# Performance work log

Hardware: AMD Instinct MI355X
Metric: run time of the kernel (lower is better)

The kernel has to match this reference:

```python
import jax, jax.numpy as jnp
import numpy as np

jax.config.update("jax_enable_x64", True)  # torch lfilter runs in double precision

SR = 24000
RES_SIZE = 64
R_MIN, R_MAX = 0.9999, 0.99999
B, T = 4, 120000


def setup_inputs() -> dict:
    # Probe coefficients (fixed buffers, computed exactly as in Probe.__init__)
    theta_min = 2 * np.pi * 10.0 / SR
    theta_max = 2 * np.pi * 100.0 / SR
    theta = np.exp(np.linspace(np.log(theta_min), np.log(theta_max), RES_SIZE))
    radii = np.linspace(R_MIN, R_MAX, RES_SIZE)
    a1 = -2.0 * radii * np.cos(theta)          # [C]
    a2 = radii ** 2                             # [C]
    b0 = (1.0 - radii) * 0.5                    # [C]

    # Tank mixing weight: orthogonal init, shape [out=64, in=128] (rows orthonormal)
    rng = np.random.default_rng(1337)
    q, _ = np.linalg.qr(rng.standard_normal((2 * RES_SIZE, RES_SIZE)))  # [128,64], orthonormal cols
    W = q.T.astype(np.float32)                  # [64,128]

    key = jax.random.key(0)
    k1, k2 = jax.random.split(key)
    pred = jax.random.normal(k1, (B, 1, T), dtype=jnp.float32)
    target = jax.random.normal(k2, (B, 1, T), dtype=jnp.float32)
    return {
        "pred": pred,
        "target": target,
        "a1": jnp.asarray(a1, jnp.float64),
        "a2": jnp.asarray(a2, jnp.float64),
        "b0": jnp.asarray(b0, jnp.float64),
        "W": jnp.asarray(W, jnp.float32),
    }


def _biquad_bank(x, a1, a2, b0):
    """Biquad filter bank. x: [N, T] float64; coeffs: [C]. Returns [N, C, T].
    y[t] = b0*x[t] - a1*y[t-1] - a2*y[t-2]  (a0 = 1, b1 = b2 = 0, clamp=False)
    """
    n = x.shape[0]
    c = a1.shape[0]

    def step(carry, xt):
        y1, y2 = carry  # each [N, C]
        y = b0[None, :] * xt[:, None] - a1[None, :] * y1 - a2[None, :] * y2
        return (y, y1), y

    init = (jnp.zeros((n, c), x.dtype), jnp.zeros((n, c), x.dtype))
    _, ys = jax.lax.scan(step, init, x.T)      # [T, N, C]
    return jnp.transpose(ys, (1, 2, 0))        # [N, C, T]


def _probe(x, a1, a2, b0):
    """x: [B,1,T] float -> [B, 2C, T] float32 (fwd state ++ bwd state)."""
    xs = x[:, 0, :].astype(jnp.float64)        # [B, T]
    # run forward-time and reversed-time filters in one batched scan
    both = jnp.concatenate([xs, xs[:, ::-1]], axis=0)       # [2B, T]
    ys = _biquad_bank(both, a1, a2, b0)                      # [2B, C, T]
    nb = xs.shape[0]
    fwd_state = ys[:nb]                                      # [B, C, T]
    bwd_state = ys[nb:][:, :, ::-1]                          # [B, C, T] (flipped back)
    return jnp.concatenate([fwd_state, bwd_state], axis=1).astype(jnp.float32)


def _tank(x, W):
    """x: [B, 2C, T], W: [C, 2C] -> tanh(W @ x): [B, C, T]."""
    return jnp.tanh(jnp.einsum("bct,oc->bot", x, W))


def reference(pred, target, a1, a2, b0, W):
    t = pred.shape[-1]
    margin = t // 3
    p_emb = _tank(_probe(pred, a1, a2, b0), W)    # [B, C, T]
    t_emb = _tank(_probe(target, a1, a2, b0), W)  # [B, C, T]
    p_valid = p_emb[..., margin:t - margin]
    t_valid = t_emb[..., margin:t - margin]
    return jnp.mean(jnp.abs(p_valid - t_valid))
```

## Files before the change

### kernel.cpp

```cpp
#include <hip/hip_runtime.h>

#define T_LEN 120000
#define LBLK 160
#define PBLK 750
#define PB_USED 500
#define SEG_LEN 25
#define NSEG_USED 20
#define SEGC0 10
#define NSEGC 11
#define CCH 32
#define NCHUNK 5
#define BATCH 4
#define K0 250
#define NKV 250
#define DENOM 20480000.0
#define YSTR 130

typedef _Float16 half8 __attribute__((ext_vector_type(8)));
typedef float f32x4 __attribute__((ext_vector_type(4)));

__device__ __forceinline__ float fast_tanh(float x) {
  float e = __expf(2.0f * x);
  return 1.0f - 2.0f / (e + 1.0f);
}

__device__ __forceinline__ bool coeffs_are_f64(const void* a2p) {
  double probe = *(const double*)a2p;
  return probe > 0.9 && probe < 1.0;
}
__device__ __forceinline__ double coeff_d(const void* p, bool f64, int ch) {
  return f64 ? ((const double*)p)[ch] : (double)((const float*)p)[ch];
}

__device__ __forceinline__ void mat_pow(double A1, double A2, int e,
                                        double& r00, double& r01,
                                        double& r10, double& r11) {
  double m00 = -A1, m01 = -A2, m10 = 1.0, m11 = 0.0;
  r00 = 1.0; r01 = 0.0; r10 = 0.0; r11 = 1.0;
  while (e) {
    if (e & 1) {
      double t00 = r00 * m00 + r01 * m10, t01 = r00 * m01 + r01 * m11;
      double t10 = r10 * m00 + r11 * m10, t11 = r10 * m01 + r11 * m11;
      r00 = t00; r01 = t01; r10 = t10; r11 = t11;
    }
    e >>= 1;
    if (e) {
      double t00 = m00 * m00 + m01 * m10, t01 = m00 * m01 + m01 * m11;
      double t10 = m10 * m00 + m11 * m10, t11 = m10 * m01 + m11 * m11;
      m00 = t00; m01 = t01; m10 = t10; m11 = t11;
    }
  }
}

__global__ __launch_bounds__(256) void pass1(
    const float* __restrict__ pred, const float* __restrict__ tgt,
    const void* a1p, const void* a2p, const void* b0p,
    double* __restrict__ fbuf, double* __restrict__ wsum)
{
  if ((blockIdx.x | blockIdx.y) == 0 && threadIdx.x == 0) {
    wsum[0] = 0.0;
    ((unsigned int*)(wsum + 1))[0] = 0u;
  }
  int k = blockIdx.x;
  int g = threadIdx.x >> 6, lane = threadIdx.x & 63;
  int gu = __builtin_amdgcn_readfirstlane(g);
  int r = blockIdx.y * 4 + gu;
  int i = r >> 3, d = (r >> 2) & 1, b = r & 3;
  const float* sig = (i ? tgt : pred) + b * T_LEN;
  __shared__ float xs[4][LBLK];
  int base = k * LBLK;
  for (int j = lane; j < LBLK; j += 64)
    xs[gu][j] = d ? sig[T_LEN - 1 - (base + j)] : sig[base + j];
  __syncthreads();
  int ch = lane;
  bool f64 = coeffs_are_f64(a2p);
  float A1 = (float)coeff_d(a1p, f64, ch);
  float A2 = (float)coeff_d(a2p, f64, ch);
  float B0 = (float)coeff_d(b0p, f64, ch);
  float y1 = 0.0f, y2 = 0.0f;
  for (int j = 0; j < LBLK; ++j) {
    float y = fmaf(-A1, y1, fmaf(-A2, y2, B0 * xs[gu][j]));
    y2 = y1; y1 = y;
  }
  int s = r * 64 + ch;
  ((double2*)fbuf)[(size_t)k * 1024 + s] = make_double2((double)y1, (double)y2);
}

__global__ __launch_bounds__(64) void pass2a(
    const void* a1p, const void* a2p,
    const double* __restrict__ fbuf, double* __restrict__ sbuf,
    double* __restrict__ atab)
{
  int seg = blockIdx.x >> 4;
  int s = ((blockIdx.x & 15) << 6) + threadIdx.x;
  int ch = s & 63;
  bool f64 = coeffs_are_f64(a2p);
  double r00, r01, r10, r11;
  mat_pow(coeff_d(a1p, f64, ch), coeff_d(a2p, f64, ch), LBLK, r00, r01, r10, r11);
  const double2* fb = (const double2*)fbuf;
  double y1 = 0.0, y2 = 0.0;
  for (int jj = 0; jj < SEG_LEN / 5; ++jj) {
    size_t kb = (size_t)(seg * SEG_LEN + jj * 5) * 1024 + s;
    double2 f0 = fb[kb], f1 = fb[kb + 1024], f2 = fb[kb + 2048],
            f3 = fb[kb + 3072], f4 = fb[kb + 4096];
    double n1, n2;
    n1 = r00*y1 + r01*y2 + f0.x; n2 = r10*y1 + r11*y2 + f0.y; y1=n1; y2=n2;
    n1 = r00*y1 + r01*y2 + f1.x; n2 = r10*y1 + r11*y2 + f1.y; y1=n1; y2=n2;
    n1 = r00*y1 + r01*y2 + f2.x; n2 = r10*y1 + r11*y2 + f2.y; y1=n1; y2=n2;
    n1 = r00*y1 + r01*y2 + f3.x; n2 = r10*y1 + r11*y2 + f3.y; y1=n1; y2=n2;
    n1 = r00*y1 + r01*y2 + f4.x; n2 = r10*y1 + r11*y2 + f4.y; y1=n1; y2=n2;
  }
  ((double2*)sbuf)[(size_t)seg * 1024 + s] = make_double2(y1, y2);

  if (blockIdx.x == 0) {
    double p00 = 1.0, p01 = 0.0, p10 = 0.0, p11 = 1.0;
    double b00 = r00, b01 = r01, b10 = r10, b11 = r11;
    int e = SEG_LEN;
    while (e) {
      if (e & 1) {
        double t00 = p00*b00 + p01*b10, t01 = p00*b01 + p01*b11;
        double t10 = p10*b00 + p11*b10, t11 = p10*b01 + p11*b11;
        p00 = t00; p01 = t01; p10 = t10; p11 = t11;
      }
      e >>= 1;
      if (e) {
        double t00 = b00*b00 + b01*b10, t01 = b00*b01 + b01*b11;
        double t10 = b10*b00 + b11*b10, t11 = b10*b01 + b11*b11;
        b00 = t00; b01 = t01; b10 = t10; b11 = t11;
      }
    }
    double* ap = atab + ch * 8;
    ap[0] = r00; ap[1] = r01; ap[2] = r10; ap[3] = r11;
    ap[4] = p00; ap[5] = p01; ap[6] = p10; ap[7] = p11;
  }
}

__global__ __launch_bounds__(64) void pass2c(
    const double* __restrict__ fbuf, const double* __restrict__ sbuf,
    const double* __restrict__ atab, double* __restrict__ stbuf)
{
  int seg = SEGC0 + (blockIdx.x >> 4);
  int s = ((blockIdx.x & 15) << 6) + threadIdx.x;
  int ch = s & 63;
  const double2* ap = (const double2*)(atab + ch * 8);
  double2 ra = ap[0], rb = ap[1], qa = ap[2], qb = ap[3];
  double r00 = ra.x, r01 = ra.y, r10 = rb.x, r11 = rb.y;
  double q00 = qa.x, q01 = qa.y, q10 = qb.x, q11 = qb.y;

  double y1 = 0.0, y2 = 0.0;
  const double2* sb = (const double2*)sbuf;
  #pragma unroll 1
  for (int qq = 0; qq < NSEG_USED; qq += 5) {
    double2 f[5];
    #pragma unroll
    for (int p = 0; p < 5; ++p) f[p] = sb[(size_t)(qq + p) * 1024 + s];
    #pragma unroll
    for (int p = 0; p < 5; ++p) {
      if (qq + p < seg) {
        double n1 = q00 * y1 + q01 * y2 + f[p].x;
        double n2 = q10 * y1 + q11 * y2 + f[p].y;
        y1 = n1; y2 = n2;
      }
    }
  }

  const double2* fb = (const double2*)fbuf;
  double2* st = (double2*)stbuf;
  #pragma unroll 1
  for (int jb = 0; jb < SEG_LEN; jb += 5) {
    double2 fv[5];
    #pragma unroll
    for (int q = 0; q < 5; ++q) {
      int m = seg * SEG_LEN + jb + q;
      int mc = m < PB_USED ? m : PB_USED - 1;
      fv[q] = fb[(size_t)mc * 1024 + s];
    }
    #pragma unroll
    for (int q = 0; q < 5; ++q) {
      int m = seg * SEG_LEN + jb + q;
      if (m <= K0 + NKV) {
        st[(size_t)(m - K0) * 1024 + s] = make_double2(y1, y2);
        if (m < K0 + NKV) {
          double n1 = r00 * y1 + r01 * y2 + fv[q].x;
          double n2 = r10 * y1 + r11 * y2 + fv[q].y;
          y1 = n1; y2 = n2;
        }
      }
    }
  }
}

__global__ __launch_bounds__(256, 4) void pass3(
    const float* __restrict__ pred, const float* __restrict__ tgt,
    const void* a1p, const void* a2p, const void* b0p,
    const float* __restrict__ W, const double* __restrict__ stbuf,
    double* __restrict__ wsum, float* __restrict__ out)
{
  int k = K0 + blockIdx.x;
  int b = blockIdx.y;
  int tid = threadIdx.x;
  __shared__ __align__(16) _Float16 ys[2][64 * YSTR];
  __shared__ float red[4];

  int g = tid >> 6, lane = tid & 63;
  int gu = __builtin_amdgcn_readfirstlane(g);
  int iu = gu >> 1, du = gu & 1;
  int ch = lane;
  int n0 = gu * 16;
  int lm = lane & 15, quad = lane >> 4;

  bool f64 = coeffs_are_f64(a2p);
  double A1d = coeff_d(a1p, f64, ch), A2d = coeff_d(a2p, f64, ch);
  double B0d = coeff_d(b0p, f64, ch);
  float A1 = (float)A1d, A2 = (float)A2d, B0 = (float)B0d;
  float IA2 = (float)(1.0 / A2d);

  int m = du ? (PBLK - k) : k;
  int s = (iu * 8 + du * 4 + b) * 64 + ch;
  double2 v0 = ((const double2*)stbuf)[(size_t)(m - K0) * 1024 + s];
  float st0 = (float)v0.x, st1 = (float)v0.y;

  half8 wf[4][4];
  #pragma unroll
  for (int m0 = 0; m0 < 4; ++m0) {
    #pragma unroll
    for (int k0 = 0; k0 < 4; ++k0) {
      const float* wp = W + (m0 * 16 + lm) * 128 + k0 * 32 + quad * 8;
      float4 wa = *(const float4*)wp, wb = *(const float4*)(wp + 4);
      half8 h;
      h[0] = (_Float16)wa.x; h[1] = (_Float16)wa.y;
      h[2] = (_Float16)wa.z; h[3] = (_Float16)wa.w;
      h[4] = (_Float16)wb.x; h[5] = (_Float16)wb.y;
      h[6] = (_Float16)wb.z; h[7] = (_Float16)wb.w;
      wf[m0][k0] = h;
    }
  }

  const float* xp = (iu ? tgt : pred) + b * T_LEN + k * LBLK;

  float loss = 0.0f;
  for (int cc = 0; cc < NCHUNK; ++cc) {
    _Float16* yb = ys[cc & 1];
    if (du == 0) {
      #pragma unroll
      for (int tt = 0; tt < CCH; ++tt) {
        float x = xp[cc * CCH + tt];
        float y = fmaf(-A1, st0, fmaf(-A2, st1, B0 * x));
        yb[(2 * tt + iu) * YSTR + ch] = (_Float16)y;
        st1 = st0; st0 = y;
      }
    } else {
      #pragma unroll
      for (int tt = 0; tt < CCH; ++tt) {
        float x = xp[cc * CCH + tt];
        yb[(2 * tt + iu) * YSTR + 64 + ch] = (_Float16)st0;
        float ym2 = (fmaf(-A1, st1, B0 * x) - st0) * IA2;
        st0 = st1; st1 = ym2;
      }
    }
    __syncthreads();

    const _Float16* yrow = &yb[(n0 + lm) * YSTR + quad * 8];
    half8 bf0 = *(const half8*)(yrow);
    half8 bf1 = *(const half8*)(yrow + 32);
    half8 bf2 = *(const half8*)(yrow + 64);
    half8 bf3 = *(const half8*)(yrow + 96);
    #pragma unroll
    for (int m0 = 0; m0 < 4; ++m0) {
      f32x4 c = {0.f, 0.f, 0.f, 0.f};
      c = __builtin_amdgcn_mfma_f32_16x16x32_f16(wf[m0][0], bf0, c, 0, 0, 0);
      c = __builtin_amdgcn_mfma_f32_16x16x32_f16(wf[m0][1], bf1, c, 0, 0, 0);
      c = __builtin_amdgcn_mfma_f32_16x16x32_f16(wf[m0][2], bf2, c, 0, 0, 0);
      c = __builtin_amdgcn_mfma_f32_16x16x32_f16(wf[m0][3], bf3, c, 0, 0, 0);
      #pragma unroll
      for (int r = 0; r < 4; ++r) {
        float vv = fast_tanh(c[r]);
        float p = __shfl_xor(vv, 1);
        loss += fabsf(vv - p);
      }
    }
  }

  #pragma unroll
  for (int off = 32; off > 0; off >>= 1) loss += __shfl_down(loss, off);
  if (lane == 0) red[g] = loss;
  __syncthreads();
  if (tid == 0) {
    float blk = (red[0] + red[1]) + (red[2] + red[3]);
    atomicAdd(wsum, (double)blk);
    __threadfence();
    unsigned int n = atomicAdd((unsigned int*)(wsum + 1), 1u);
    if (n == (unsigned int)(NKV * BATCH - 1)) {
      __threadfence();
      double tot = atomicAdd(wsum, 0.0);
      out[0] = (float)(tot / DENOM);
    }
  }
}

extern "C" void kernel_launch(void* const* d_in, const int* in_sizes, int n_in,
                              void* d_out, int out_size, void* d_ws, size_t ws_size,
                              hipStream_t stream) {
  const float* pred = (const float*)d_in[0];
  const float* tgt  = (const float*)d_in[1];
  const void* a1p = d_in[2];
  const void* a2p = d_in[3];
  const void* b0p = d_in[4];
  const float* W  = (const float*)d_in[5];
  float* out = (float*)d_out;

  double* base = (double*)d_ws;
  double* wsum = base;
  double* fbuf = base + 8;
  double* sbuf = fbuf + (size_t)PB_USED * 1024 * 2;
  double* atab = sbuf + (size_t)32 * 1024 * 2;
  double* stbuf = atab + 512;

  pass1<<<dim3(PB_USED, 4), 256, 0, stream>>>(pred, tgt, a1p, a2p, b0p,
                                              fbuf, wsum);
  pass2a<<<NSEG_USED * 16, 64, 0, stream>>>(a1p, a2p, fbuf, sbuf, atab);
  pass2c<<<NSEGC * 16, 64, 0, stream>>>(fbuf, sbuf, atab, stbuf);
  pass3<<<dim3(NKV, BATCH), 256, 0, stream>>>(pred, tgt, a1p, a2p, b0p,
                                              W, stbuf, wsum, out);
}
```

Measured before the change: 128.7 us.

## Merge segment-scan passes and replace atomic loss reduction with finalize kernel

Removes the pass2a kernel that computed per-segment carries and the R^25 powers. pass2c now serially scans all block carries in its prefix (up to ~500 sequential steps per thread) using only the 160-step transition matrix, which removes one launch and the sbuf/atab traffic. The atomic accumulation with a last-block counter in pass3 is replaced by per-block partial sums written to memory and reduced by a separate single-block finalize kernel. The trade-off is a much longer serial dependency chain in pass2c and one extra kernel launch, in exchange for dropping one launch and the atomics.

```diff
diff --git a/kernel.cpp b/kernel.cpp
--- a/kernel.cpp
+++ b/kernel.cpp
@@ -5,7 +5,6 @@
 #define PBLK 750
 #define PB_USED 500
 #define SEG_LEN 25
-#define NSEG_USED 20
 #define SEGC0 10
 #define NSEGC 11
 #define CCH 32
@@ -55,12 +54,8 @@
 __global__ __launch_bounds__(256) void pass1(
     const float* __restrict__ pred, const float* __restrict__ tgt,
     const void* a1p, const void* a2p, const void* b0p,
-    double* __restrict__ fbuf, double* __restrict__ wsum)
-{
-  if ((blockIdx.x | blockIdx.y) == 0 && threadIdx.x == 0) {
-    wsum[0] = 0.0;
-    ((unsigned int*)(wsum + 1))[0] = 0u;
-  }
+    double* __restrict__ fbuf)
+{
   int k = blockIdx.x;
   int g = threadIdx.x >> 6, lane = threadIdx.x & 63;
   int gu = __builtin_amdgcn_readfirstlane(g);
@@ -86,101 +81,50 @@
   ((double2*)fbuf)[(size_t)k * 1024 + s] = make_double2((double)y1, (double)y2);
 }
 
-__global__ __launch_bounds__(64) void pass2a(
+__global__ __launch_bounds__(64) void pass2c(
     const void* a1p, const void* a2p,
-    const double* __restrict__ fbuf, double* __restrict__ sbuf,
-    double* __restrict__ atab)
-{
-  int seg = blockIdx.x >> 4;
+    const double* __restrict__ fbuf, double* __restrict__ stbuf)
+{
+  int seg = SEGC0 + (blockIdx.x >> 4);
   int s = ((blockIdx.x & 15) << 6) + threadIdx.x;
   int ch = s & 63;
   bool f64 = coeffs_are_f64(a2p);
   double r00, r01, r10, r11;
-  mat_pow(coeff_d(a1p, f64, ch), coeff_d(a2p, f64, ch), LBLK, r00, r01, r10, r11);
+  mat_pow(coeff_d(a1p, f64, ch), coeff_d(a2p, f64, ch), LBLK,
+          r00, r01, r10, r11);
   const double2* fb = (const double2*)fbuf;
+
   double y1 = 0.0, y2 = 0.0;
-  for (int jj = 0; jj < SEG_LEN / 5; ++jj) {
-    size_t kb = (size_t)(seg * SEG_LEN + jj * 5) * 1024 + s;
-    double2 f0 = fb[kb], f1 = fb[kb + 1024], f2 = fb[kb + 2048],
-            f3 = fb[kb + 3072], f4 = fb[kb + 4096];
-    double n1, n2;
-    n1 = r00*y1 + r01*y2 + f0.x; n2 = r10*y1 + r11*y2 + f0.y; y1=n1; y2=n2;
-    n1 = r00*y1 + r01*y2 + f1.x; n2 = r10*y1 + r11*y2 + f1.y; y1=n1; y2=n2;
-    n1 = r00*y1 + r01*y2 + f2.x; n2 = r10*y1 + r11*y2 + f2.y; y1=n1; y2=n2;
-    n1 = r00*y1 + r01*y2 + f3.x; n2 = r10*y1 + r11*y2 + f3.y; y1=n1; y2=n2;
-    n1 = r00*y1 + r01*y2 + f4.x; n2 = r10*y1 + r11*y2 + f4.y; y1=n1; y2=n2;
-  }
-  ((double2*)sbuf)[(size_t)seg * 1024 + s] = make_double2(y1, y2);
-
-  if (blockIdx.x == 0) {
-    double p00 = 1.0, p01 = 0.0, p10 = 0.0, p11 = 1.0;
-    double b00 = r00, b01 = r01, b10 = r10, b11 = r11;
-    int e = SEG_LEN;
-    while (e) {
-      if (e & 1) {
-        double t00 = p00*b00 + p01*b10, t01 = p00*b01 + p01*b11;
-        double t10 = p10*b00 + p11*b10, t11 = p10*b01 + p11*b11;
-        p00 = t00; p01 = t01; p10 = t10; p11 = t11;
-      }
-      e >>= 1;
-      if (e) {
-        double t00 = b00*b00 + b01*b10, t01 = b00*b01 + b01*b11;
-        double t10 = b10*b00 + b11*b10, t11 = b10*b01 + b11*b11;
-        b00 = t00; b01 = t01; b10 = t10; b11 = t11;
-      }
-    }
-    double* ap = atab + ch * 8;
-    ap[0] = r00; ap[1] = r01; ap[2] = r10; ap[3] = r11;
-    ap[4] = p00; ap[5] = p01; ap[6] = p10; ap[7] = p11;
-  }
-}
-
-__global__ __launch_bounds__(64) void pass2c(
-    const double* __restrict__ fbuf, const double* __restrict__ sbuf,
-    const double* __restrict__ atab, double* __restrict__ stbuf)
-{
-  int seg = SEGC0 + (blockIdx.x >> 4);
-  int s = ((blockIdx.x & 15) << 6) + threadIdx.x;
-  int ch = s & 63;
-  const double2* ap = (const double2*)(atab + ch * 8);
-  double2 ra = ap[0], rb = ap[1], qa = ap[2], qb = ap[3];
-  double r00 = ra.x, r01 = ra.y, r10 = rb.x, r11 = rb.y;
-  double q00 = qa.x, q01 = qa.y, q10 = qb.x, q11 = qb.y;
-
-  double y1 = 0.0, y2 = 0.0;
-  const double2* sb = (const double2*)sbuf;
+  int pref = seg * SEG_LEN;
   #pragma unroll 1
-  for (int qq = 0; qq < NSEG_USED; qq += 5) {
+  for (int mb = 0; mb < pref; mb += 5) {
     double2 f[5];
     #pragma unroll
-    for (int p = 0; p < 5; ++p) f[p] = sb[(size_t)(qq + p) * 1024 + s];
-    #pragma unroll
-    for (int p = 0; p < 5; ++p) {
-      if (qq + p < seg) {
-        double n1 = q00 * y1 + q01 * y2 + f[p].x;
-        double n2 = q10 * y1 + q11 * y2 + f[p].y;
-        y1 = n1; y2 = n2;
-      }
-    }
-  }
-
-  const double2* fb = (const double2*)fbuf;
+    for (int q = 0; q < 5; ++q) f[q] = fb[(size_t)(mb + q) * 1024 + s];
+    #pragma unroll
+    for (int q = 0; q < 5; ++q) {
+      double n1 = r00 * y1 + r01 * y2 + f[q].x;
+      double n2 = r10 * y1 + r11 * y2 + f[q].y;
+      y1 = n1; y2 = n2;
+    }
+  }
+
   double2* st = (double2*)stbuf;
   #pragma unroll 1
   for (int jb = 0; jb < SEG_LEN; jb += 5) {
     double2 fv[5];
     #pragma unroll
     for (int q = 0; q < 5; ++q) {
-      int m = seg * SEG_LEN + jb + q;
-      int mc = m < PB_USED ? m : PB_USED - 1;
+      int m2 = pref + jb + q;
+      int mc = m2 < PB_USED ? m2 : PB_USED - 1;
       fv[q] = fb[(size_t)mc * 1024 + s];
     }
     #pragma unroll
     for (int q = 0; q < 5; ++q) {
-      int m = seg * SEG_LEN + jb + q;
-      if (m <= K0 + NKV) {
-        st[(size_t)(m - K0) * 1024 + s] = make_double2(y1, y2);
-        if (m < K0 + NKV) {
+      int m2 = pref + jb + q;
+      if (m2 <= K0 + NKV) {
+        st[(size_t)(m2 - K0) * 1024 + s] = make_double2(y1, y2);
+        if (m2 < K0 + NKV) {
           double n1 = r00 * y1 + r01 * y2 + fv[q].x;
           double n2 = r10 * y1 + r11 * y2 + fv[q].y;
           y1 = n1; y2 = n2;
@@ -194,7 +138,7 @@
     const float* __restrict__ pred, const float* __restrict__ tgt,
     const void* a1p, const void* a2p, const void* b0p,
     const float* __restrict__ W, const double* __restrict__ stbuf,
-    double* __restrict__ wsum, float* __restrict__ out)
+    double* __restrict__ partial)
 {
   int k = K0 + blockIdx.x;
   int b = blockIdx.y;
@@ -285,17 +229,24 @@
   for (int off = 32; off > 0; off >>= 1) loss += __shfl_down(loss, off);
   if (lane == 0) red[g] = loss;
   __syncthreads();
-  if (tid == 0) {
-    float blk = (red[0] + red[1]) + (red[2] + red[3]);
-    atomicAdd(wsum, (double)blk);
-    __threadfence();
-    unsigned int n = atomicAdd((unsigned int*)(wsum + 1), 1u);
-    if (n == (unsigned int)(NKV * BATCH - 1)) {
-      __threadfence();
-      double tot = atomicAdd(wsum, 0.0);
-      out[0] = (float)(tot / DENOM);
-    }
-  }
+  if (tid == 0)
+    partial[b * NKV + blockIdx.x] =
+        (double)((red[0] + red[1]) + (red[2] + red[3]));
+}
+
+__global__ __launch_bounds__(256) void finalize(
+    const double* __restrict__ partial, float* __restrict__ out)
+{
+  __shared__ double dred[4];
+  int tid = threadIdx.x, lane = tid & 63, g = tid >> 6;
+  double v = partial[tid] + partial[tid + 256] + partial[tid + 512];
+  if (tid + 768 < NKV * BATCH) v += partial[tid + 768];
+  #pragma unroll
+  for (int off = 32; off > 0; off >>= 1) v += __shfl_down(v, off);
+  if (lane == 0) dred[g] = v;
+  __syncthreads();
+  if (tid == 0)
+    out[0] = (float)(((dred[0] + dred[1]) + (dred[2] + dred[3])) / DENOM);
 }
 
 extern "C" void kernel_launch(void* const* d_in, const int* in_sizes, int n_in,
@@ -310,16 +261,13 @@
   float* out = (float*)d_out;
 
   double* base = (double*)d_ws;
-  double* wsum = base;
-  double* fbuf = base + 8;
-  double* sbuf = fbuf + (size_t)PB_USED * 1024 * 2;
-  double* atab = sbuf + (size_t)32 * 1024 * 2;
-  double* stbuf = atab + 512;
-
-  pass1<<<dim3(PB_USED, 4), 256, 0, stream>>>(pred, tgt, a1p, a2p, b0p,
-                                              fbuf, wsum);
-  pass2a<<<NSEG_USED * 16, 64, 0, stream>>>(a1p, a2p, fbuf, sbuf, atab);
-  pass2c<<<NSEGC * 16, 64, 0, stream>>>(fbuf, sbuf, atab, stbuf);
+  double* fbuf = base;
+  double* stbuf = fbuf + (size_t)PB_USED * 1024 * 2;
+  double* partial = stbuf + (size_t)(NKV + 1) * 1024 * 2;
+
+  pass1<<<dim3(PB_USED, 4), 256, 0, stream>>>(pred, tgt, a1p, a2p, b0p, fbuf);
+  pass2c<<<NSEGC * 16, 64, 0, stream>>>(a1p, a2p, fbuf, stbuf);
   pass3<<<dim3(NKV, BATCH), 256, 0, stream>>>(pred, tgt, a1p, a2p, b0p,
-                                              W, stbuf, wsum, out);
-}
+                                              W, stbuf, partial);
+  finalize<<<1, 256, 0, stream>>>(partial, out);
+}
```

After: 146.4 us. 13.7% more time.
